# Kernel tuning notes

Hardware: AMD Instinct MI355X
Metric: run time of the kernel (lower is better)

The kernel has to match this reference:

```python
import jax, jax.numpy as jnp
import numpy as np


def setup_inputs() -> dict:
    key = jax.random.key(0)
    k1, k2, k3, k4 = jax.random.split(key, 4)
    n = 1000000
    nnz = 18000000
    ncols = 8
    field = jax.random.normal(k1, (n, ncols), dtype=jnp.float32)
    lap_vals = jax.random.normal(k2, (nnz,), dtype=jnp.float32)
    lap_row = jax.random.randint(k3, (nnz,), 0, n, dtype=jnp.int32).astype(jnp.int64)
    lap_col = jax.random.randint(k4, (nnz,), 0, n, dtype=jnp.int32).astype(jnp.int64)
    return {"field": field, "lap_vals": lap_vals, "lap_row": lap_row,
            "lap_col": lap_col, "n_vertices": n}


def reference(field, lap_vals, lap_row, lap_col, n_vertices):
    """Apply sparse Laplacian (COO, duplicates summed) to all field columns at once.

    Equivalent to torch.sparse.mm(L, field) where L = coo(row, col, vals, (n, n)).
    One fused gather-multiply-scatter pass replaces the per-column loop.
    """
    field = field.astype(jnp.float32)
    # gather: [nnz, ncols]
    contrib = lap_vals[:, None] * field[lap_col]
    # scatter-add over rows: [n, ncols]
    out = jax.ops.segment_sum(contrib, lap_row, num_segments=n_vertices)
    return out
```

## Files before the change

kernel.cpp:

```cpp
#include <hip/hip_runtime.h>

#define NCOLS  8
#define BLOCK  256
#define NB     512
#define NBKT   1024
#define LG2RPB 10
#define RPB    1024
#define NCB    32
#define NCHUNK 16
#define CB     (NB / NCHUNK)
#define CAP    23040

__device__ __forceinline__ int detect_is64(const void* p) {
    const unsigned* w = (const unsigned*)p;
    int is64 = 1;
    #pragma unroll
    for (int k = 0; k < 16; ++k) is64 &= (w[2 * k + 1] == 0u) ? 1 : 0;
    return is64;
}

__device__ __forceinline__ int load_idx(const void* p, int i, int is64) {
    return is64 ? (int)((const long long*)p)[i] : ((const int*)p)[i];
}

__global__ __launch_bounds__(BLOCK) void k_hist(
    const void* __restrict__ rowp, int nnz, int chunk, unsigned* __restrict__ hist)
{
    __shared__ unsigned h[NBKT];
    const int is64 = detect_is64(rowp);
    for (int i = threadIdx.x; i < NBKT; i += BLOCK) h[i] = 0u;
    __syncthreads();
    const int beg = blockIdx.x * chunk;
    const int end = min(nnz, beg + chunk);
    for (int i = beg + threadIdx.x; i < end; i += BLOCK)
        atomicAdd(&h[load_idx(rowp, i, is64) >> LG2RPB], 1u);
    __syncthreads();
    unsigned* row = hist + (size_t)blockIdx.x * NBKT;
    for (int i = threadIdx.x; i < NBKT; i += BLOCK) row[i] = h[i];
}

__global__ __launch_bounds__(BLOCK) void k_partial(
    const unsigned* __restrict__ hist, unsigned* __restrict__ partial)
{
    const int t = blockIdx.x * BLOCK + threadIdx.x;
    const int c = t >> 10, k = t & (NBKT - 1);
    unsigned s = 0;
    #pragma unroll 4
    for (int j = 0; j < CB; ++j) s += hist[(size_t)(c * CB + j) * NBKT + k];
    partial[(size_t)c * NBKT + k] = s;
}

__global__ __launch_bounds__(NBKT) void k_scan(
    unsigned* __restrict__ partial, unsigned* __restrict__ base)
{
    __shared__ unsigned s[NBKT];
    const int k = threadIdx.x;
    unsigned tot = 0;
    #pragma unroll
    for (int c = 0; c < NCHUNK; ++c) tot += partial[(size_t)c * NBKT + k];
    s[k] = tot;
    __syncthreads();
    for (int off = 1; off < NBKT; off <<= 1) {
        unsigned v = (k >= off) ? s[k - off] : 0u;
        __syncthreads();
        s[k] += v;
        __syncthreads();
    }
    unsigned run = s[k] - tot;
    base[k] = run;
    if (k == NBKT - 1) base[NBKT] = s[k];
    #pragma unroll
    for (int c = 0; c < NCHUNK; ++c) {
        unsigned t = partial[(size_t)c * NBKT + k];
        partial[(size_t)c * NBKT + k] = run;
        run += t;
    }
}

__global__ __launch_bounds__(BLOCK) void k_apply(
    unsigned* __restrict__ hist, const unsigned* __restrict__ partial)
{
    const int t = blockIdx.x * BLOCK + threadIdx.x;
    const int c = t >> 10, k = t & (NBKT - 1);
    unsigned run = partial[(size_t)c * NBKT + k];
    #pragma unroll 4
    for (int j = 0; j < CB; ++j) {
        const size_t idx = (size_t)(c * CB + j) * NBKT + k;
        unsigned v = hist[idx];
        hist[idx] = run;
        run += v;
    }
}

__global__ __launch_bounds__(BLOCK) void k_scatter(
    const float* __restrict__ vals, const void* __restrict__ rowp,
    const void* __restrict__ colp, int nnz, int chunk,
    const unsigned* __restrict__ hist, uint2* __restrict__ records)
{
    __shared__ unsigned cur[NBKT];
    const int is64 = detect_is64(rowp);
    const unsigned* wb = hist + (size_t)blockIdx.x * NBKT;
    for (int i = threadIdx.x; i < NBKT; i += BLOCK) cur[i] = wb[i];
    __syncthreads();
    const int beg = blockIdx.x * chunk;
    const int end = min(nnz, beg + chunk);
    for (int i = beg + threadIdx.x; i < end; i += BLOCK) {
        int r = load_idx(rowp, i, is64);
        int c = load_idx(colp, i, is64);
        float v = vals[i];
        unsigned pos = atomicAdd(&cur[r >> LG2RPB], 1u);
        records[pos] = make_uint2((((unsigned)r & (RPB - 1u)) << 20) | (unsigned)c,
                                  __float_as_uint(v));
    }
}

__global__ __launch_bounds__(BLOCK) void k_accum3(
    const uint2* __restrict__ records, const unsigned* __restrict__ base,
    const float* __restrict__ field, float* __restrict__ out, int n, int lg2cpb)
{
    __shared__ float acc[NCOLS * RPB];
    __shared__ unsigned short sidx[CAP];
    __shared__ unsigned cnt[NCB];
    __shared__ unsigned cur[NCB];

    const int b = blockIdx.x;
    const unsigned beg = base[b], end = base[b + 1];
    const unsigned m = end - beg;

    for (int i = threadIdx.x; i < NCOLS * RPB; i += BLOCK) acc[i] = 0.f;
    if (threadIdx.x < NCB) cnt[threadIdx.x] = 0u;
    __syncthreads();

    if (m <= CAP) {
        for (unsigned i = threadIdx.x; i < m; i += BLOCK) {
            unsigned cb = (records[beg + i].x & 0xFFFFFu) >> lg2cpb;
            atomicAdd(&cnt[cb], 1u);
        }
        __syncthreads();
        if (threadIdx.x == 0) {
            unsigned run = 0;
            #pragma unroll
            for (int k = 0; k < NCB; ++k) { cur[k] = run; run += cnt[k]; }
        }
        __syncthreads();
        for (unsigned i = threadIdx.x; i < m; i += BLOCK) {
            unsigned cb = (records[beg + i].x & 0xFFFFFu) >> lg2cpb;
            sidx[atomicAdd(&cur[cb], 1u)] = (unsigned short)i;
        }
        __syncthreads();
        for (unsigned i = threadIdx.x; i < m; i += BLOCK) {
            const uint2 rec = records[beg + sidx[i]];
            const unsigned col = rec.x & 0xFFFFFu;
            const unsigned lr  = rec.x >> 20;
            const float v = __uint_as_float(rec.y);
            const float4* f = (const float4*)(field + (size_t)col * NCOLS);
            const float4 f0 = f[0], f1 = f[1];
            atomicAdd(&acc[0 * RPB + lr], v * f0.x);
            atomicAdd(&acc[1 * RPB + lr], v * f0.y);
            atomicAdd(&acc[2 * RPB + lr], v * f0.z);
            atomicAdd(&acc[3 * RPB + lr], v * f0.w);
            atomicAdd(&acc[4 * RPB + lr], v * f1.x);
            atomicAdd(&acc[5 * RPB + lr], v * f1.y);
            atomicAdd(&acc[6 * RPB + lr], v * f1.z);
            atomicAdd(&acc[7 * RPB + lr], v * f1.w);
        }
    } else {
        for (unsigned i = beg + threadIdx.x; i < end; i += BLOCK) {
            const uint2 rec = records[i];
            const unsigned col = rec.x & 0xFFFFFu;
            const unsigned lr  = rec.x >> 20;
            const float v = __uint_as_float(rec.y);
            const float4* f = (const float4*)(field + (size_t)col * NCOLS);
            const float4 f0 = f[0], f1 = f[1];
            atomicAdd(&acc[0 * RPB + lr], v * f0.x);
            atomicAdd(&acc[1 * RPB + lr], v * f0.y);
            atomicAdd(&acc[2 * RPB + lr], v * f0.z);
            atomicAdd(&acc[3 * RPB + lr], v * f0.w);
            atomicAdd(&acc[4 * RPB + lr], v * f1.x);
            atomicAdd(&acc[5 * RPB + lr], v * f1.y);
            atomicAdd(&acc[6 * RPB + lr], v * f1.z);
            atomicAdd(&acc[7 * RPB + lr], v * f1.w);
        }
    }
    __syncthreads();

    const size_t row0 = (size_t)b * RPB;
    for (int t = threadIdx.x; t < NCOLS * RPB; t += BLOCK) {
        int r = t >> 3, j = t & 7;
        size_t gr = row0 + (size_t)r;
        if (gr < (size_t)n) out[gr * NCOLS + j] = acc[j * RPB + r];
    }
}

__global__ __launch_bounds__(BLOCK) void lap_zero_kernel(float4* __restrict__ out, int n4) {
    int i = blockIdx.x * BLOCK + threadIdx.x;
    if (i < n4) out[i] = make_float4(0.f, 0.f, 0.f, 0.f);
}

__global__ __launch_bounds__(BLOCK) void lap_spmm_atomic(
    const float* __restrict__ vals, const void* __restrict__ rowp,
    const void* __restrict__ colp, const float* __restrict__ field,
    float* __restrict__ out, int nnz)
{
    const int is64 = detect_is64(rowp);
    int i = blockIdx.x * BLOCK + threadIdx.x;
    if (i >= nnz) return;
    float v = vals[i];
    int r = load_idx(rowp, i, is64);
    int c = load_idx(colp, i, is64);
    const float4* f = (const float4*)(field + (size_t)c * NCOLS);
    float4 f0 = f[0], f1 = f[1];
    float* o = out + (size_t)r * NCOLS;
    unsafeAtomicAdd(o + 0, v * f0.x);
    unsafeAtomicAdd(o + 1, v * f0.y);
    unsafeAtomicAdd(o + 2, v * f0.z);
    unsafeAtomicAdd(o + 3, v * f0.w);
    unsafeAtomicAdd(o + 4, v * f1.x);
    unsafeAtomicAdd(o + 5, v * f1.y);
    unsafeAtomicAdd(o + 6, v * f1.z);
    unsafeAtomicAdd(o + 7, v * f1.w);
}

extern "C" void kernel_launch(void* const* d_in, const int* in_sizes, int n_in,
                              void* d_out, int out_size, void* d_ws, size_t ws_size,
                              hipStream_t stream) {
    const float* field = (const float*)d_in[0];
    const float* vals  = (const float*)d_in[1];
    const void*  rowp  = d_in[2];
    const void*  colp  = d_in[3];
    float* out = (float*)d_out;

    const int nnz = in_sizes[1];
    const int n   = out_size / NCOLS;
    char* ws = (char*)d_ws;

    const size_t o_hist    = 0;
    const size_t o_partial = o_hist + (size_t)NB * NBKT * 4;
    const size_t o_base    = o_partial + (size_t)NCHUNK * NBKT * 4;
    const size_t o_rec     = (o_base + (size_t)(NBKT + 1) * 4 + 255) & ~(size_t)255;
    const size_t need      = o_rec + (size_t)nnz * 8;

    if (n <= NBKT * RPB && n <= (1 << 20) && ws_size >= need) {
        unsigned* hist    = (unsigned*)(ws + o_hist);
        unsigned* partial = (unsigned*)(ws + o_partial);
        unsigned* base    = (unsigned*)(ws + o_base);
        uint2*    rec     = (uint2*)(ws + o_rec);

        const int chunk = (nnz + NB - 1) / NB;

        int lg = 0;
        while ((1u << lg) < (unsigned)n) ++lg;
        const int lg2cpb = lg > 5 ? lg - 5 : 0;

        k_hist<<<NB, BLOCK, 0, stream>>>(rowp, nnz, chunk, hist);
        k_partial<<<NCHUNK * NBKT / BLOCK, BLOCK, 0, stream>>>(hist, partial);
        k_scan<<<1, NBKT, 0, stream>>>(partial, base);
        k_apply<<<NCHUNK * NBKT / BLOCK, BLOCK, 0, stream>>>(hist, partial);
        k_scatter<<<NB, BLOCK, 0, stream>>>(vals, rowp, colp, nnz, chunk, hist, rec);
        k_accum3<<<NBKT, BLOCK, 0, stream>>>(rec, base, field, out, n, lg2cpb);
        return;
    }

    const int n4 = out_size / 4;
    lap_zero_kernel<<<(n4 + BLOCK - 1) / BLOCK, BLOCK, 0, stream>>>((float4*)out, n4);
    lap_spmm_atomic<<<(nnz + BLOCK - 1) / BLOCK, BLOCK, 0, stream>>>(
        vals, rowp, colp, field, out, nnz);
}
```

Measured before the change: 1.360 ms.

## Split accumulation into column-slice passes after in-place slice sort of records

Adds a kernel that sorts each row bucket's records in place into 8 column-range slices, using shared memory, and writes per-slice offsets. Accumulation then runs as 8 sequential launches, each gathering field rows from only one eighth of the column space, so the gathered working set fits better in L2/LLC. The cost is a re-read and re-write of the records, eight passes that load and store the output tile, and extra kernel launches.

```diff
diff --git a/kernel.cpp b/kernel.cpp
--- a/kernel.cpp
+++ b/kernel.cpp
@@ -1,15 +1,15 @@
 #include <hip/hip_runtime.h>
 
-#define NCOLS  8
-#define BLOCK  256
-#define NB     512
-#define NBKT   1024
-#define LG2RPB 10
-#define RPB    1024
-#define NCB    32
-#define NCHUNK 16
-#define CB     (NB / NCHUNK)
-#define CAP    23040
+#define NCOLS   8
+#define BLOCK   256
+#define NB      512
+#define NBKT    1024
+#define LG2RPB  10
+#define RPB     1024
+#define NCHUNK  16
+#define CB      (NB / NCHUNK)
+#define NSLICE  8
+#define SORTCAP 19456
 
 __device__ __forceinline__ int detect_is64(const void* p) {
     const unsigned* w = (const unsigned*)p;
@@ -114,77 +114,102 @@
     }
 }
 
-__global__ __launch_bounds__(BLOCK) void k_accum3(
-    const uint2* __restrict__ records, const unsigned* __restrict__ base,
-    const float* __restrict__ field, float* __restrict__ out, int n, int lg2cpb)
+__global__ __launch_bounds__(BLOCK) void k_slicesort(
+    uint2* __restrict__ records, const unsigned* __restrict__ base,
+    unsigned* __restrict__ boff, int lg2spl)
+{
+    __shared__ uint2 buf[SORTCAP];
+    __shared__ unsigned short cnt[BLOCK][NSLICE];
+    __shared__ unsigned sbase[NSLICE + 1];
+    const int b = blockIdx.x, t = threadIdx.x;
+    const unsigned beg = base[b], end = base[b + 1], m = end - beg;
+
+    if (m > SORTCAP) {
+        if (t < NSLICE) boff[b * NSLICE + t] = t ? end : beg;
+        return;
+    }
+
+    unsigned short c[NSLICE];
+    #pragma unroll
+    for (int s = 0; s < NSLICE; ++s) c[s] = 0;
+    for (unsigned i = t; i < m; i += BLOCK)
+        c[(records[beg + i].x & 0xFFFFFu) >> lg2spl]++;
+    #pragma unroll
+    for (int s = 0; s < NSLICE; ++s) cnt[t][s] = c[s];
+    __syncthreads();
+
+    if (t < NSLICE) {
+        unsigned run = 0;
+        for (int k = 0; k < BLOCK; ++k) {
+            unsigned v = cnt[k][t];
+            cnt[k][t] = (unsigned short)run;
+            run += v;
+        }
+        sbase[t] = run;
+    }
+    __syncthreads();
+    if (t == 0) {
+        unsigned run = 0;
+        #pragma unroll
+        for (int s = 0; s < NSLICE; ++s) { unsigned v = sbase[s]; sbase[s] = run; run += v; }
+        sbase[NSLICE] = run;
+    }
+    __syncthreads();
+    if (t < NSLICE) boff[b * NSLICE + t] = beg + sbase[t];
+
+    unsigned cur[NSLICE];
+    #pragma unroll
+    for (int s = 0; s < NSLICE; ++s) cur[s] = sbase[s] + cnt[t][s];
+    for (unsigned i = t; i < m; i += BLOCK) {
+        uint2 r = records[beg + i];
+        unsigned s = (r.x & 0xFFFFFu) >> lg2spl;
+        buf[cur[s]++] = r;
+    }
+    __syncthreads();
+
+    for (unsigned i = t; i < m; i += BLOCK) records[beg + i] = buf[i];
+}
+
+__global__ __launch_bounds__(BLOCK) void k_accum_s(
+    const uint2* __restrict__ records, const unsigned* __restrict__ boff,
+    const unsigned* __restrict__ base, const float* __restrict__ field,
+    float* __restrict__ out, int n, int s)
 {
     __shared__ float acc[NCOLS * RPB];
-    __shared__ unsigned short sidx[CAP];
-    __shared__ unsigned cnt[NCB];
-    __shared__ unsigned cur[NCB];
-
     const int b = blockIdx.x;
-    const unsigned beg = base[b], end = base[b + 1];
-    const unsigned m = end - beg;
-
-    for (int i = threadIdx.x; i < NCOLS * RPB; i += BLOCK) acc[i] = 0.f;
-    if (threadIdx.x < NCB) cnt[threadIdx.x] = 0u;
-    __syncthreads();
-
-    if (m <= CAP) {
-        for (unsigned i = threadIdx.x; i < m; i += BLOCK) {
-            unsigned cb = (records[beg + i].x & 0xFFFFFu) >> lg2cpb;
-            atomicAdd(&cnt[cb], 1u);
+    const size_t row0 = (size_t)b * RPB;
+
+    if (s == 0) {
+        for (int i = threadIdx.x; i < NCOLS * RPB; i += BLOCK) acc[i] = 0.f;
+    } else {
+        for (int t = threadIdx.x; t < NCOLS * RPB; t += BLOCK) {
+            int r = t >> 3, j = t & 7;
+            size_t gr = row0 + (size_t)r;
+            acc[j * RPB + r] = (gr < (size_t)n) ? out[gr * NCOLS + j] : 0.f;
         }
-        __syncthreads();
-        if (threadIdx.x == 0) {
-            unsigned run = 0;
-            #pragma unroll
-            for (int k = 0; k < NCB; ++k) { cur[k] = run; run += cnt[k]; }
-        }
-        __syncthreads();
-        for (unsigned i = threadIdx.x; i < m; i += BLOCK) {
-            unsigned cb = (records[beg + i].x & 0xFFFFFu) >> lg2cpb;
-            sidx[atomicAdd(&cur[cb], 1u)] = (unsigned short)i;
-        }
-        __syncthreads();
-        for (unsigned i = threadIdx.x; i < m; i += BLOCK) {
-            const uint2 rec = records[beg + sidx[i]];
-            const unsigned col = rec.x & 0xFFFFFu;
-            const unsigned lr  = rec.x >> 20;
-            const float v = __uint_as_float(rec.y);
-            const float4* f = (const float4*)(field + (size_t)col * NCOLS);
-            const float4 f0 = f[0], f1 = f[1];
-            atomicAdd(&acc[0 * RPB + lr], v * f0.x);
-            atomicAdd(&acc[1 * RPB + lr], v * f0.y);
-            atomicAdd(&acc[2 * RPB + lr], v * f0.z);
-            atomicAdd(&acc[3 * RPB + lr], v * f0.w);
-            atomicAdd(&acc[4 * RPB + lr], v * f1.x);
-            atomicAdd(&acc[5 * RPB + lr], v * f1.y);
-            atomicAdd(&acc[6 * RPB + lr], v * f1.z);
-            atomicAdd(&acc[7 * RPB + lr], v * f1.w);
-        }
-    } else {
-        for (unsigned i = beg + threadIdx.x; i < end; i += BLOCK) {
-            const uint2 rec = records[i];
-            const unsigned col = rec.x & 0xFFFFFu;
-            const unsigned lr  = rec.x >> 20;
-            const float v = __uint_as_float(rec.y);
-            const float4* f = (const float4*)(field + (size_t)col * NCOLS);
-            const float4 f0 = f[0], f1 = f[1];
-            atomicAdd(&acc[0 * RPB + lr], v * f0.x);
-            atomicAdd(&acc[1 * RPB + lr], v * f0.y);
-            atomicAdd(&acc[2 * RPB + lr], v * f0.z);
-            atomicAdd(&acc[3 * RPB + lr], v * f0.w);
-            atomicAdd(&acc[4 * RPB + lr], v * f1.x);
-            atomicAdd(&acc[5 * RPB + lr], v * f1.y);
-            atomicAdd(&acc[6 * RPB + lr], v * f1.z);
-            atomicAdd(&acc[7 * RPB + lr], v * f1.w);
-        }
-    }
-    __syncthreads();
-
-    const size_t row0 = (size_t)b * RPB;
+    }
+    __syncthreads();
+
+    const unsigned sbeg = boff[b * NSLICE + s];
+    const unsigned send = (s < NSLICE - 1) ? boff[b * NSLICE + s + 1] : base[b + 1];
+    for (unsigned i = sbeg + threadIdx.x; i < send; i += BLOCK) {
+        const uint2 rec = records[i];
+        const unsigned col = rec.x & 0xFFFFFu;
+        const unsigned lr  = rec.x >> 20;
+        const float v = __uint_as_float(rec.y);
+        const float4* f = (const float4*)(field + (size_t)col * NCOLS);
+        const float4 f0 = f[0], f1 = f[1];
+        atomicAdd(&acc[0 * RPB + lr], v * f0.x);
+        atomicAdd(&acc[1 * RPB + lr], v * f0.y);
+        atomicAdd(&acc[2 * RPB + lr], v * f0.z);
+        atomicAdd(&acc[3 * RPB + lr], v * f0.w);
+        atomicAdd(&acc[4 * RPB + lr], v * f1.x);
+        atomicAdd(&acc[5 * RPB + lr], v * f1.y);
+        atomicAdd(&acc[6 * RPB + lr], v * f1.z);
+        atomicAdd(&acc[7 * RPB + lr], v * f1.w);
+    }
+    __syncthreads();
+
     for (int t = threadIdx.x; t < NCOLS * RPB; t += BLOCK) {
         int r = t >> 3, j = t & 7;
         size_t gr = row0 + (size_t)r;
@@ -242,6 +267,7 @@
 
     if (n <= NBKT * RPB && n <= (1 << 20) && ws_size >= need) {
         unsigned* hist    = (unsigned*)(ws + o_hist);
+        unsigned* boff    = (unsigned*)(ws + o_hist);
         unsigned* partial = (unsigned*)(ws + o_partial);
         unsigned* base    = (unsigned*)(ws + o_base);
         uint2*    rec     = (uint2*)(ws + o_rec);
@@ -250,14 +276,16 @@
 
         int lg = 0;
         while ((1u << lg) < (unsigned)n) ++lg;
-        const int lg2cpb = lg > 5 ? lg - 5 : 0;
+        const int lg2spl = lg > 3 ? lg - 3 : 0;
 
         k_hist<<<NB, BLOCK, 0, stream>>>(rowp, nnz, chunk, hist);
         k_partial<<<NCHUNK * NBKT / BLOCK, BLOCK, 0, stream>>>(hist, partial);
         k_scan<<<1, NBKT, 0, stream>>>(partial, base);
         k_apply<<<NCHUNK * NBKT / BLOCK, BLOCK, 0, stream>>>(hist, partial);
         k_scatter<<<NB, BLOCK, 0, stream>>>(vals, rowp, colp, nnz, chunk, hist, rec);
-        k_accum3<<<NBKT, BLOCK, 0, stream>>>(rec, base, field, out, n, lg2cpb);
+        k_slicesort<<<NBKT, BLOCK, 0, stream>>>(rec, base, boff, lg2spl);
+        for (int s = 0; s < NSLICE; ++s)
+            k_accum_s<<<NBKT, BLOCK, 0, stream>>>(rec, boff, base, field, out, n, s);
         return;
     }
 
```

Result: slower. 1.647 ms (+21.2%).
